# Optimization experiments

Measured on AMD Instinct MI355X. Metric: run time of the kernel, lower is better.

The kernel has to match this reference:

```python
import jax, jax.numpy as jnp
import numpy as np

EPS_KERAS = 1e-7  # keras backend epsilon used by SparseCategoricalCrossentropy clipping


def _box_terms(p_boxes, g_boxes):
    # boxes are cxcywh; module uses pixel-style '+1' widths. Returns (iou, bg_ratio).
    p_ul = p_boxes[..., :2] - 0.5 * p_boxes[..., 2:]
    p_dr = p_boxes[..., :2] + 0.5 * p_boxes[..., 2:]
    g_ul = g_boxes[..., :2] - 0.5 * g_boxes[..., 2:]
    g_dr = g_boxes[..., :2] + 0.5 * g_boxes[..., 2:]
    inter_wh = jnp.maximum(jnp.minimum(p_dr, g_dr) - jnp.maximum(p_ul, g_ul) + 1.0, 0.0)
    inter = inter_wh[..., 0] * inter_wh[..., 1]
    p_wh = jnp.maximum(p_dr - p_ul + 1.0, 0.0)
    g_wh = jnp.maximum(g_dr - g_ul + 1.0, 0.0)
    p_area = p_wh[..., 0] * p_wh[..., 1]
    g_area = g_wh[..., 0] * g_wh[..., 1]
    union = p_area + g_area - inter
    iou = inter / jnp.maximum(union, 1e-9)
    bound_wh = jnp.maximum(jnp.maximum(p_dr, g_dr) - jnp.minimum(p_ul, g_ul) + 1.0, 0.0)
    bound = bound_wh[..., 0] * bound_wh[..., 1]
    bg_ratio = (bound - union) / jnp.maximum(bound, 1e-9)
    return iou, bg_ratio


def _cost_matrix(bbox_pred, labels_pred, bbox_gt, labels_gt):
    # Vectorized over batch: [B,Q,G] pairwise L1 + (-GIoU) + (-prob of gt class)
    bp = bbox_pred[:, :, None, :]   # [B,Q,1,4]
    bg = bbox_gt[:, None, :, :]     # [B,1,G,4]
    l1 = jnp.sum(jnp.abs(bp - bg), axis=-1)
    iou, bg_ratio = _box_terms(bp, bg)
    B, Q, _ = labels_pred.shape
    G = labels_gt.shape[1]
    idx = jnp.broadcast_to(labels_gt[:, None, :].astype(jnp.int32), (B, Q, G))
    probs = jnp.take_along_axis(labels_pred, idx, axis=2)
    return l1 - (iou - bg_ratio) - probs


def _hungarian(cost):
    # Exact min-cost assignment for a square matrix (Jonker-Volgenant style,
    # e-maxx Hungarian). Host-side, mirrors scipy.optimize.linear_sum_assignment.
    cost = np.asarray(cost, dtype=np.float64)
    n = cost.shape[0]
    u = np.zeros(n + 1)
    v = np.zeros(n + 1)
    p = np.zeros(n + 1, dtype=np.int64)    # p[j]: row matched to column j (1-based)
    way = np.zeros(n + 1, dtype=np.int64)
    for i in range(1, n + 1):
        p[0] = i
        j0 = 0
        minv = np.full(n + 1, np.inf)
        used = np.zeros(n + 1, dtype=bool)
        while True:
            used[j0] = True
            i0 = p[j0]
            cur = cost[i0 - 1] - u[i0] - v[1:]
            free = ~used[1:]
            better = free & (cur < minv[1:])
            minv[1:][better] = cur[better]
            way[1:][better] = j0
            masked = np.where(free, minv[1:], np.inf)
            j1 = int(np.argmin(masked)) + 1
            delta = masked[j1 - 1]
            uidx = np.nonzero(used)[0]
            u[p[uidx]] += delta
            v[uidx] -= delta
            minv[~used] -= delta
            j0 = j1
            if p[j0] == 0:
                break
        while j0 != 0:
            j1 = way[j0]
            p[j0] = p[j1]
            j0 = j1
    ans = np.zeros(n, dtype=np.int64)
    ans[p[1:] - 1] = np.arange(n)   # ans[row] = matched col
    return ans


def _losses(bbox_pred, labels_pred, bbox_gt, labels_gt, col):
    # col: [B,Q] matched gt column per query (row_ind is arange for square cost).
    # Label loss: scatter of matched gt labels onto queries == gather by col,
    # then keras SparseCategoricalCrossentropy(from_logits=False):
    # clip probs to [eps,1-eps], log, softmax-CE (== -log p for normalized probs).
    query_labels = jnp.take_along_axis(labels_gt.astype(jnp.int32), col, axis=1)  # [B,Q]
    logits = jnp.log(jnp.clip(labels_pred, EPS_KERAS, 1.0 - EPS_KERAS))
    logp = jax.nn.log_softmax(logits, axis=-1)
    nll = -jnp.take_along_axis(logp, query_labels[..., None], axis=-1)[..., 0]    # [B,Q]
    label_loss = jnp.mean(nll, axis=1)
    # Bbox L1: pred rows gathered by arange (identity), gt gathered by col.
    target = jnp.take_along_axis(bbox_gt, col[..., None], axis=1)                 # [B,Q,4]
    reg_loss = jnp.mean(jnp.abs(bbox_pred - target), axis=(1, 2))
    # GIoU term: original code uses UN-permuted gt here (faithful to source),
    # and adds +mean(iou - bg_ratio) (sign as in source).
    iou, bg_ratio = _box_terms(bbox_pred, bbox_gt)
    giou = jnp.mean(iou - bg_ratio, axis=1)
    per_sample = 1.0 * label_loss + 5.0 * reg_loss + 2.0 * giou
    return jnp.sum(per_sample)


def reference(bbox_pred, labels_pred, bbox_gt, labels_gt):
    cost = np.asarray(_cost_matrix(bbox_pred, labels_pred, bbox_gt, labels_gt))
    col = jnp.asarray(np.stack([_hungarian(c) for c in cost]))  # [B,Q]
    return _losses(bbox_pred, labels_pred, bbox_gt, labels_gt, col)


def setup_inputs() -> dict:
    key = jax.random.key(0)
    k1, k2, k3, k4 = jax.random.split(key, 4)
    B, Q, G, C = 16, 100, 100, 100
    bbox_pred = jax.random.uniform(k1, (B, Q, 4), dtype=jnp.float32)
    labels_pred = jax.nn.softmax(jax.random.normal(k2, (B, Q, C), dtype=jnp.float32), axis=-1)
    bbox_gt = jax.random.uniform(k3, (B, G, 4), dtype=jnp.float32)
    labels_gt = jax.random.randint(k4, (B, G), 0, C, dtype=jnp.int32)
    return {"bbox_pred": bbox_pred, "labels_pred": labels_pred, "bbox_gt": bbox_gt, "labels_gt": labels_gt}
```

## Files before the change

kernel.cpp:

```cpp
#include <hip/hip_runtime.h>
#include <math.h>

#define NB 100

__device__ __forceinline__ void box_terms(const float bp[4], const float bg[4],
                                          float &iou, float &bgr) {
    float p_ul0 = bp[0] - 0.5f * bp[2], p_ul1 = bp[1] - 0.5f * bp[3];
    float p_dr0 = bp[0] + 0.5f * bp[2], p_dr1 = bp[1] + 0.5f * bp[3];
    float g_ul0 = bg[0] - 0.5f * bg[2], g_ul1 = bg[1] - 0.5f * bg[3];
    float g_dr0 = bg[0] + 0.5f * bg[2], g_dr1 = bg[1] + 0.5f * bg[3];
    float iw0 = fmaxf(fminf(p_dr0, g_dr0) - fmaxf(p_ul0, g_ul0) + 1.0f, 0.0f);
    float iw1 = fmaxf(fminf(p_dr1, g_dr1) - fmaxf(p_ul1, g_ul1) + 1.0f, 0.0f);
    float inter = iw0 * iw1;
    float pw0 = fmaxf(p_dr0 - p_ul0 + 1.0f, 0.0f);
    float pw1 = fmaxf(p_dr1 - p_ul1 + 1.0f, 0.0f);
    float gw0 = fmaxf(g_dr0 - g_ul0 + 1.0f, 0.0f);
    float gw1 = fmaxf(g_dr1 - g_ul1 + 1.0f, 0.0f);
    float pa = pw0 * pw1, ga = gw0 * gw1;
    float uni = pa + ga - inter;
    iou = inter / fmaxf(uni, 1e-9f);
    float bw0 = fmaxf(fmaxf(p_dr0, g_dr0) - fminf(p_ul0, g_ul0) + 1.0f, 0.0f);
    float bw1 = fmaxf(fmaxf(p_dr1, g_dr1) - fminf(p_ul1, g_ul1) + 1.0f, 0.0f);
    float bound = bw0 * bw1;
    bgr = (bound - uni) / fmaxf(bound, 1e-9f);
}

template<int CTRL>
__device__ __forceinline__ double dpp_f64(double x) {
    int lo = __builtin_amdgcn_update_dpp(0, __double2loint(x), CTRL, 0xF, 0xF, true);
    int hi = __builtin_amdgcn_update_dpp(0, __double2hiint(x), CTRL, 0xF, 0xF, true);
    return __hiloint2double(hi, lo);
}

template<int CTRL>
__device__ __forceinline__ double dpp_f64_keep(double x) {
    int lo = __builtin_amdgcn_update_dpp(__double2loint(x), __double2loint(x),
                                         CTRL, 0xF, 0xF, false);
    int hi = __builtin_amdgcn_update_dpp(__double2hiint(x), __double2hiint(x),
                                         CTRL, 0xF, 0xF, false);
    return __hiloint2double(hi, lo);
}

__device__ __forceinline__ double readlane_f64(double x, int l) {
    int lo = __builtin_amdgcn_readlane(__double2loint(x), l);
    int hi = __builtin_amdgcn_readlane(__double2hiint(x), l);
    return __hiloint2double(hi, lo);
}

__device__ __forceinline__ double wave_min_f64(double x) {
    double q1 = dpp_f64<0xB1>(x);
    double q2 = dpp_f64<0x4E>(x);
    double q3 = dpp_f64<0x1B>(x);
    x = fmin(fmin(x, q1), fmin(q2, q3));
    double h1 = dpp_f64<0x141>(x);
    double h2 = dpp_f64<0x140>(x);
    double h3 = dpp_f64_keep<0x118>(x);
    x = fmin(fmin(x, h1), fmin(h2, h3));
    x = fmin(x, dpp_f64<0x142>(x));
    x = fmin(x, dpp_f64<0x143>(x));
    return readlane_f64(x, 63);
}

__device__ __forceinline__ double wave_min_packed(double x, int &lo_out) {
    double q1 = dpp_f64<0xB1>(x);
    double q2 = dpp_f64<0x4E>(x);
    double q3 = dpp_f64<0x1B>(x);
    x = fmin(fmin(x, q1), fmin(q2, q3));
    double h1 = dpp_f64<0x141>(x);
    double h2 = dpp_f64<0x140>(x);
    double h3 = dpp_f64_keep<0x118>(x);
    x = fmin(fmin(x, h1), fmin(h2, h3));
    x = fmin(x, dpp_f64<0x142>(x));
    x = fmin(x, dpp_f64<0x143>(x));
    int lo = __builtin_amdgcn_readlane(__double2loint(x), 63);
    int hi = __builtin_amdgcn_readlane(__double2hiint(x), 63);
    lo_out = lo;
    return __hiloint2double(hi, lo);
}

__device__ __forceinline__ double pack_tag(double g, int tag) {
    unsigned long long bi = (unsigned long long)__double_as_longlong(g);
    bi = (bi & ~0x3FFFULL) | (unsigned long long)(unsigned)tag;
    return __longlong_as_double((long long)bi);
}

__global__ __launch_bounds__(256) void fused_match_loss(
    const float* __restrict__ bbox_pred,
    const float* __restrict__ labels_pred,
    const float* __restrict__ bbox_gt,
    const int*   __restrict__ labels_gt,
    float* __restrict__ out)
{
    __shared__ float  cost_sh[NB * NB + 64];
    __shared__ double u_sh[NB];
    __shared__ double v_sh[NB];
    __shared__ int    rowclaim_sh[NB];
    __shared__ int    col_sh[NB];
    __shared__ float  bp_sh[NB * 4];
    __shared__ float  bg_sh[NB * 4];
    __shared__ int    lg_sh[NB];
    __shared__ float  red_sh[3 * 128];

    const int b = blockIdx.x;
    const int t = threadIdx.x;
    const int lane = t & 63;
    const bool hasB = (lane + 64 < NB);
    const double INF = (double)INFINITY;
    const double QNAN = __longlong_as_double(0x7FF8000000000000LL);
    const float* lp = labels_pred + (size_t)b * NB * NB;

    double vA = 0.0, vB = 0.0;
    double uA = 0.0, uB = 0.0;
    int pA = -1, pB = -1;
    unsigned long long remLo = 0, remHi = 0;

    for (int i = t; i < NB * 4; i += 256) {
        bp_sh[i] = bbox_pred[(size_t)b * NB * 4 + i];
        bg_sh[i] = bbox_gt[(size_t)b * NB * 4 + i];
    }
    for (int i = t; i < NB; i += 256) {
        lg_sh[i] = labels_gt[b * NB + i];
        rowclaim_sh[i] = 0x7FFFFFFF;
    }
    __syncthreads();

    for (int idx = t; idx < NB * NB; idx += 256) {
        int q = idx / NB, g = idx - q * NB;
        float bp[4] = {bp_sh[q*4+0], bp_sh[q*4+1], bp_sh[q*4+2], bp_sh[q*4+3]};
        float bg[4] = {bg_sh[g*4+0], bg_sh[g*4+1], bg_sh[g*4+2], bg_sh[g*4+3]};
        float l1 = fabsf(bp[0]-bg[0]) + fabsf(bp[1]-bg[1])
                 + fabsf(bp[2]-bg[2]) + fabsf(bp[3]-bg[3]);
        float iou, bgr;
        box_terms(bp, bg, iou, bgr);
        float prob = lp[q * NB + lg_sh[g]];
        cost_sh[idx] = l1 - (iou - bgr) - prob;
    }
    __syncthreads();

    if (t < 64) {
        float bestA = INFINITY, bestB = INFINITY;
        int iminA = 0, iminB = 0;
        for (int i = 0; i < NB; ++i) {
            float cA = cost_sh[i * NB + lane];
            float cB = cost_sh[i * NB + lane + 64];
            if (cA < bestA) { bestA = cA; iminA = i; }
            if (hasB && cB < bestB) { bestB = cB; iminB = i; }
        }
        atomicMin(&rowclaim_sh[iminA], lane);
        if (hasB) atomicMin(&rowclaim_sh[iminB], lane + 64);

        vA = (double)bestA;
        vB = hasB ? (double)bestB : 0.0;
        v_sh[lane] = vA;
        if (hasB) v_sh[lane + 64] = vB;
        pA = (rowclaim_sh[iminA] == lane) ? iminA : -1;
        pB = (hasB && rowclaim_sh[iminB] == lane + 64) ? iminB : -1;
        remLo = __ballot(rowclaim_sh[lane] == 0x7FFFFFFF);
        remHi = __ballot(hasB && rowclaim_sh[lane + 64] == 0x7FFFFFFF);
    }
    __syncthreads();

    {
        const int w = t >> 6;
        for (int i = w; i < NB; i += 4) {
            double r = (double)cost_sh[i * NB + lane] - v_sh[lane];
            if (hasB)
                r = fmin(r, (double)cost_sh[i * NB + lane + 64] - v_sh[lane + 64]);
            r = wave_min_f64(r);
            if (lane == 0)
                u_sh[i] = (rowclaim_sh[i] != 0x7FFFFFFF) ? 0.0 : r;
        }
    }
    __syncthreads();

    if (t < 64) {
        {
            unsigned long long gLo = remLo, gHi = remHi;
            while (gLo | gHi) {
                int i;
                if (gLo) { i = __ffsll((long long)gLo) - 1; gLo &= gLo - 1; }
                else { i = 64 + __ffsll((long long)gHi) - 1; gHi &= gHi - 1; }
                double u_i = u_sh[i];
                const float* crow = &cost_sh[i * NB];
                double rdA = (double)crow[lane] - u_i - vA;
                double rdB = (double)crow[lane + 64] - u_i - vB;
                unsigned long long ba = __ballot(pA < 0 && rdA == 0.0);
                unsigned long long bb = __ballot(hasB && pB < 0 && rdB == 0.0);
                if (ba) {
                    int wl = __ffsll((long long)ba) - 1;
                    if (lane == wl) { pA = i; uA = u_i; }
                } else if (bb) {
                    int wl = __ffsll((long long)bb) - 1;
                    if (lane == wl) { pB = i; uB = u_i; }
                } else continue;
                if (i < 64) remLo &= ~(1ull << i); else remHi &= ~(1ull << (i - 64));
            }
        }

        auto phase = [&](int irow) {
            double GAq = QNAN, GBq = QNAN;
            int wayA = -1, wayB = -1;
            bool usedA = false, usedB = !hasB;
            double DusedA = 0.0, DusedB = 0.0;
            double D = 0.0;
            int jprevmark = -1;
            double u0 = u_sh[irow];
            double Df; int jfin;

            const int tagA = ((pA + 1) << 7) | lane;
            const int tagB = ((pB + 1) << 7) | (lane + 64);

            float cA = cost_sh[irow * NB + lane];
            float cB = cost_sh[irow * NB + lane + 64];

            for (;;) {
                double du = D - u0;
                double candAq = pack_tag(((double)cA - vA) + du, tagA);
                if (!usedA && !(candAq >= GAq)) { GAq = candAq; wayA = jprevmark; }
                double candBq = pack_tag(((double)cB - vB) + du, tagB);
                if (!usedB && !(candBq >= GBq)) { GBq = candBq; wayB = jprevmark; }
                int wlo;
                const double m = wave_min_packed(fmin(GAq, GBq), wlo);
                const int j1 = wlo & 0x7F;
                const int prow = ((wlo >> 7) & 0x7F) - 1;
                const bool isA = (j1 < 64);
                const int winLane = j1 & 63;
                if (prow < 0) { Df = m; jfin = j1; break; }
                cA = cost_sh[prow * NB + lane];
                cB = cost_sh[prow * NB + lane + 64];
                double unext = readlane_f64(isA ? uA : uB, winLane);
                if (lane == winLane) {
                    if (isA) { usedA = true; DusedA = m; GAq = QNAN; }
                    else     { usedB = true; DusedB = m; GBq = QNAN; }
                }
                u0 = unext; jprevmark = j1; D = m;
            }

            if (usedA) { uA += Df - DusedA; vA -= Df - DusedA; }
            if (hasB && usedB) { uB += Df - DusedB; vB -= Df - DusedB; }

            int jcur = jfin;
            while (jcur != -1) {
                int wl = jcur & 63;
                int jprev = (jcur < 64) ? __builtin_amdgcn_readlane(wayA, wl)
                                        : __builtin_amdgcn_readlane(wayB, wl);
                int row; double unew;
                if (jprev < 0) { row = irow; unew = u_sh[irow] + Df; }
                else {
                    int pl = jprev & 63;
                    int rA = __builtin_amdgcn_readlane(pA, pl);
                    int rB = __builtin_amdgcn_readlane(pB, pl);
                    double xA = readlane_f64(uA, pl);
                    double xB = readlane_f64(uB, pl);
                    row  = (jprev < 64) ? rA : rB;
                    unew = (jprev < 64) ? xA : xB;
                }
                if (jcur < 64) { if (lane == jcur)      { pA = row; uA = unew; } }
                else           { if (lane == jcur - 64) { pB = row; uB = unew; } }
                jcur = jprev;
            }
        };

        while (remLo) { int i = __ffsll((long long)remLo) - 1; remLo &= remLo - 1; phase(i); }
        while (remHi) { int i = 64 + __ffsll((long long)remHi) - 1; remHi &= remHi - 1; phase(i); }

        if (pA >= 0) col_sh[pA] = lane;
        if (hasB && pB >= 0) col_sh[pB] = lane + 64;
    }
    __syncthreads();

    float nll = 0.0f, regsum = 0.0f, giou = 0.0f;
    if (t < NB) {
        const int q = t;
        const int cg = col_sh[q];
        const int cidx = lg_sh[cg];
        const float* row = lp + q * NB;
        const float hi = 1.0f - 1e-7f;
        float mx = -INFINITY;
        for (int k = 0; k < NB; ++k) {
            float lg = logf(fminf(fmaxf(row[k], 1e-7f), hi));
            mx = fmaxf(mx, lg);
        }
        float se = 0.0f, logit_c = 0.0f;
        for (int k = 0; k < NB; ++k) {
            float lg = logf(fminf(fmaxf(row[k], 1e-7f), hi));
            se += expf(lg - mx);
            if (k == cidx) logit_c = lg;
        }
        nll = (mx + logf(se)) - logit_c;

        for (int k = 0; k < 4; ++k)
            regsum += fabsf(bp_sh[q*4+k] - bg_sh[cg*4+k]);

        float bp[4] = {bp_sh[q*4+0], bp_sh[q*4+1], bp_sh[q*4+2], bp_sh[q*4+3]};
        float bq[4] = {bg_sh[q*4+0], bg_sh[q*4+1], bg_sh[q*4+2], bg_sh[q*4+3]};
        float iou, bgr;
        box_terms(bp, bq, iou, bgr);
        giou = iou - bgr;
    }
    if (t < 128) {
        red_sh[t]       = nll;
        red_sh[128 + t] = regsum;
        red_sh[256 + t] = giou;
    }
    __syncthreads();
    if (t < 64) {
        float a = red_sh[t]       + red_sh[t + 64];
        float r = red_sh[128 + t] + red_sh[128 + t + 64];
        float g = red_sh[256 + t] + red_sh[256 + t + 64];
        #pragma unroll
        for (int off = 32; off > 0; off >>= 1) {
            a += __shfl_xor(a, off, 64);
            r += __shfl_xor(r, off, 64);
            g += __shfl_xor(g, off, 64);
        }
        if (t == 0) {
            float ps = a * (1.0f / NB) + 5.0f * (r * (1.0f / (NB * 4)))
                     + 2.0f * (g * (1.0f / NB));
            atomicAdd(out, ps);
        }
    }
}

extern "C" void kernel_launch(void* const* d_in, const int* in_sizes, int n_in,
                              void* d_out, int out_size, void* d_ws, size_t ws_size,
                              hipStream_t stream) {
    const float* bbox_pred   = (const float*)d_in[0];
    const float* labels_pred = (const float*)d_in[1];
    const float* bbox_gt     = (const float*)d_in[2];
    const int*   labels_gt   = (const int*)d_in[3];
    float* out = (float*)d_out;

    const int B = in_sizes[0] / (NB * 4);

    fused_match_loss<<<B, 256, 0, stream>>>(bbox_pred, labels_pred, bbox_gt,
                                            labels_gt, out);
}
```

Measured before the change: 366.5 us.

## Overlap log-sum-exp and GIoU with Hungarian wave; split min-reduction off the dependency chain

The matching-independent parts of the loss (per-row log-sum-exp over class probabilities and the unpermuted GIoU term) now run on the idle waves (threads 64+) while wave 0 runs the serial Hungarian search. After the sync, only the matched class logit and the L1 term are computed. The inner augmenting loop is also reworked. It starts the wave-min over the old minima before the candidate update, does a second wave-min over the new candidates, and combines the two, so the first reduction no longer waits on the candidate computation. This doubles the cross-lane reductions per step, and tie-breaking between the two minima may differ subtly from before.

```diff
diff --git a/kernel.cpp b/kernel.cpp
--- a/kernel.cpp
+++ b/kernel.cpp
@@ -99,13 +99,14 @@
     __shared__ float  bp_sh[NB * 4];
     __shared__ float  bg_sh[NB * 4];
     __shared__ int    lg_sh[NB];
+    __shared__ float  lse_sh[NB];
+    __shared__ float  gio_sh[NB];
     __shared__ float  red_sh[3 * 128];
 
     const int b = blockIdx.x;
     const int t = threadIdx.x;
     const int lane = t & 63;
     const bool hasB = (lane + 64 < NB);
-    const double INF = (double)INFINITY;
     const double QNAN = __longlong_as_double(0x7FF8000000000000LL);
     const float* lp = labels_pred + (size_t)b * NB * NB;
 
@@ -214,13 +215,19 @@
             float cB = cost_sh[irow * NB + lane + 64];
 
             for (;;) {
+                int wloG;
+                double mG = wave_min_packed(fmin(GAq, GBq), wloG);
                 double du = D - u0;
-                double candAq = pack_tag(((double)cA - vA) + du, tagA);
-                if (!usedA && !(candAq >= GAq)) { GAq = candAq; wayA = jprevmark; }
-                double candBq = pack_tag(((double)cB - vB) + du, tagB);
-                if (!usedB && !(candBq >= GBq)) { GBq = candBq; wayB = jprevmark; }
-                int wlo;
-                const double m = wave_min_packed(fmin(GAq, GBq), wlo);
+                double candA = pack_tag(((double)cA - vA) + du, tagA);
+                double candB = pack_tag(((double)cB - vB) + du, tagB);
+                double candAm = usedA ? QNAN : candA;
+                double candBm = usedB ? QNAN : candB;
+                int wloC;
+                double mC = wave_min_packed(fmin(candAm, candBm), wloC);
+                double m = fmin(mG, mC);
+                int wlo = (m == mC) ? wloC : wloG;
+                if (!usedA && !(candA >= GAq)) { GAq = candA; wayA = jprevmark; }
+                if (!usedB && !(candB >= GBq)) { GBq = candB; wayB = jprevmark; }
                 const int j1 = wlo & 0x7F;
                 const int prow = ((wlo >> 7) & 0x7F) - 1;
                 const bool isA = (j1 < 64);
@@ -266,6 +273,29 @@
 
         if (pA >= 0) col_sh[pA] = lane;
         if (hasB && pB >= 0) col_sh[pB] = lane + 64;
+    } else {
+        const int q = t - 64;
+        if (q < NB) {
+            const float* row = lp + q * NB;
+            const float hi = 1.0f - 1e-7f;
+            float mx = -INFINITY;
+            for (int k = 0; k < NB; ++k) {
+                float lg = logf(fminf(fmaxf(row[k], 1e-7f), hi));
+                mx = fmaxf(mx, lg);
+            }
+            float se = 0.0f;
+            for (int k = 0; k < NB; ++k) {
+                float lg = logf(fminf(fmaxf(row[k], 1e-7f), hi));
+                se += expf(lg - mx);
+            }
+            lse_sh[q] = mx + logf(se);
+
+            float bp[4] = {bp_sh[q*4+0], bp_sh[q*4+1], bp_sh[q*4+2], bp_sh[q*4+3]};
+            float bq[4] = {bg_sh[q*4+0], bg_sh[q*4+1], bg_sh[q*4+2], bg_sh[q*4+3]};
+            float iou, bgr;
+            box_terms(bp, bq, iou, bgr);
+            gio_sh[q] = iou - bgr;
+        }
     }
     __syncthreads();
 
@@ -274,29 +304,14 @@
         const int q = t;
         const int cg = col_sh[q];
         const int cidx = lg_sh[cg];
-        const float* row = lp + q * NB;
         const float hi = 1.0f - 1e-7f;
-        float mx = -INFINITY;
-        for (int k = 0; k < NB; ++k) {
-            float lg = logf(fminf(fmaxf(row[k], 1e-7f), hi));
-            mx = fmaxf(mx, lg);
-        }
-        float se = 0.0f, logit_c = 0.0f;
-        for (int k = 0; k < NB; ++k) {
-            float lg = logf(fminf(fmaxf(row[k], 1e-7f), hi));
-            se += expf(lg - mx);
-            if (k == cidx) logit_c = lg;
-        }
-        nll = (mx + logf(se)) - logit_c;
+        float logit_c = logf(fminf(fmaxf(lp[q * NB + cidx], 1e-7f), hi));
+        nll = lse_sh[q] - logit_c;
 
         for (int k = 0; k < 4; ++k)
             regsum += fabsf(bp_sh[q*4+k] - bg_sh[cg*4+k]);
 
-        float bp[4] = {bp_sh[q*4+0], bp_sh[q*4+1], bp_sh[q*4+2], bp_sh[q*4+3]};
-        float bq[4] = {bg_sh[q*4+0], bg_sh[q*4+1], bg_sh[q*4+2], bg_sh[q*4+3]};
-        float iou, bgr;
-        box_terms(bp, bq, iou, bgr);
-        giou = iou - bgr;
+        giou = gio_sh[q];
     }
     if (t < 128) {
         red_sh[t]       = nll;
```

Result: slower. 426.2 us (+16.3%).
